# Optimization experiments

Hardware: AMD Instinct MI355X
Metric: run time of the kernel (lower is better)

Reference implementation:

```python
import jax, jax.numpy as jnp
import numpy as np

HEADS = 16
DIM_HEAD = 64
SCALE = DIM_HEAD ** -0.5


def setup_inputs() -> dict:
    key = jax.random.key(0)
    k1, k2, k3, k4 = jax.random.split(key, 4)
    b, n, dim = 2, 2048, 1024
    inner = HEADS * DIM_HEAD  # 1024
    x = jax.random.normal(k1, (b, n, dim), dtype=jnp.float32)
    # binary keep-mask (multiplicative, as in the original module)
    seq_mask = (jax.random.uniform(k2, (b, n)) < 0.9).astype(jnp.float32)
    # weights stored [in, out] (transpose of torch Linear layout)
    w_qkv = jax.random.normal(k3, (dim, inner * 3), dtype=jnp.float32) * (dim ** -0.5)
    w_out = jax.random.normal(k4, (inner, dim), dtype=jnp.float32) * (inner ** -0.5)
    return {"x": x, "seq_mask": seq_mask, "w_qkv": w_qkv, "w_out": w_out}


def reference(x, seq_mask, w_qkv, w_out):
    b, n, dim = x.shape
    qkv = x @ w_qkv                                   # [b, n, 3*inner]
    q, k, v = jnp.split(qkv, 3, axis=-1)
    split_heads = lambda t: t.reshape(b, n, HEADS, DIM_HEAD).transpose(0, 2, 1, 3)
    q, k, v = split_heads(q), split_heads(k), split_heads(v)  # [b, h, n, d]
    dots = jnp.einsum('bhid,bhjd->bhij', q, k) * SCALE        # [b, h, n, n]
    # multiplicative mask, broadcast over heads and query index i; mask depends on key index j
    dots = dots * seq_mask[:, None, None, :]
    attn = jax.nn.softmax(dots, axis=-1)
    out = jnp.einsum('bhij,bhjd->bhid', attn, v)              # [b, h, n, d]
    out = out.transpose(0, 2, 1, 3).reshape(b, n, HEADS * DIM_HEAD)
    return out @ w_out                                        # dropout p=0 -> identity
```

## Files before the change

### kernel.cpp

```cpp
#include <hip/hip_runtime.h>
#include <hip/hip_bf16.h>

using bf16 = __hip_bfloat16;
typedef __attribute__((ext_vector_type(8))) short short8;
typedef __attribute__((ext_vector_type(4))) float floatx4;
typedef __attribute__((ext_vector_type(16))) float floatx16;

#define MFMA_BF16(a, b, c) __builtin_amdgcn_mfma_f32_16x16x32_bf16((a), (b), (c), 0, 0, 0)
#define MFMA32(a, b, c) __builtin_amdgcn_mfma_f32_32x32x16_bf16((a), (b), (c), 0, 0, 0)

__device__ __forceinline__ void gload_lds16(const bf16* g, bf16* l) {
  __builtin_amdgcn_global_load_lds((__attribute__((address_space(1))) void*)g,
                                   (__attribute__((address_space(3))) void*)l,
                                   16, 0, 0);
}

__device__ __forceinline__ unsigned short bfbits(float f) {
  bf16 b = __float2bfloat16(f);
  return *reinterpret_cast<unsigned short*>(&b);
}

__device__ __forceinline__ int swz32(int r) { return (r & 7) ^ ((r >> 3) & 3); }

#define KSCALE 0.18033688011112042f

__global__ __launch_bounds__(256)
void probemask_k(const void* __restrict__ msrc, bf16* __restrict__ dst,
                 int* __restrict__ flag) {
  __shared__ int any;
  const int tid = threadIdx.x;
  if (tid == 0) any = 0;
  __syncthreads();
  const unsigned* mw = (const unsigned*)msrc;
  int bad = 0;
#pragma unroll
  for (int i = 0; i < 4; i++) {
    unsigned w = mw[tid * 4 + i];
    if (w != 0u && w != 0x3F800000u) bad = 1;
  }
  if (bad) atomicOr(&any, 1);
  __syncthreads();
  const int isbf = any;
  if (tid == 0) flag[0] = isbf;
  if (isbf) {
#pragma unroll
    for (int i = 0; i < 2; i++)
      ((int4*)dst)[tid * 2 + i] = ((const int4*)msrc)[tid * 2 + i];
  } else {
#pragma unroll
    for (int i = 0; i < 4; i++) {
      float4 v = ((const float4*)msrc)[tid * 4 + i];
      int o = tid * 16 + i * 4;
      dst[o + 0] = __float2bfloat16(v.x);
      dst[o + 1] = __float2bfloat16(v.y);
      dst[o + 2] = __float2bfloat16(v.z);
      dst[o + 3] = __float2bfloat16(v.w);
    }
  }
}

__global__ __launch_bounds__(256)
void cvt_k(const void* __restrict__ src, bf16* __restrict__ dst, int n,
           const int* __restrict__ flag) {
  if (*flag) return;
  int i = (blockIdx.x * 256 + threadIdx.x) * 4;
  if (i >= n) return;
  float4 v = ((const float4*)src)[i >> 2];
  dst[i + 0] = __float2bfloat16(v.x);
  dst[i + 1] = __float2bfloat16(v.y);
  dst[i + 2] = __float2bfloat16(v.z);
  dst[i + 3] = __float2bfloat16(v.w);
}

__global__ __launch_bounds__(256)
void transpose2_k(const void* __restrict__ in0, bf16* __restrict__ out0,
                  const void* __restrict__ in1, bf16* __restrict__ out1,
                  const int* __restrict__ flag) {
  __shared__ bf16 tile[32][33];
  const int isbf = *flag;
  constexpr int R = 1024;
  const void* in;
  bf16* out;
  int C, bx;
  if (blockIdx.x < 96) { in = in0; out = out0; C = 3072; bx = blockIdx.x * 32; }
  else                 { in = in1; out = out1; C = 1024; bx = (blockIdx.x - 96) * 32; }
  int by = blockIdx.y * 32;
  int tx = threadIdx.x & 31, ty = threadIdx.x >> 5;
#pragma unroll
  for (int i = 0; i < 4; i++) {
    size_t idx = (size_t)(by + ty + i * 8) * C + bx + tx;
    tile[ty + i * 8][tx] =
        isbf ? ((const bf16*)in)[idx] : __float2bfloat16(((const float*)in)[idx]);
  }
  __syncthreads();
#pragma unroll
  for (int i = 0; i < 4; i++)
    out[(size_t)(bx + ty + i * 8) * R + by + tx] = tile[tx][ty + i * 8];
}

template <int MODE>
__global__ __launch_bounds__(256, 2)
void gemm_k(const bf16* __restrict__ A, const bf16* __restrict__ Aalt,
            const bf16* __restrict__ Bt,
            bf16* __restrict__ Qo, bf16* __restrict__ Ko, bf16* __restrict__ Vo,
            void* __restrict__ Co, const bf16* __restrict__ Mk,
            const int* __restrict__ flag) {
  constexpr int K = 1024;
  __shared__ __align__(16) bf16 As[128 * 32];
  __shared__ __align__(16) bf16 Bs[128 * 32];

  const int tid = threadIdx.x;
  const int lane = tid & 63;
  const int wv = tid >> 6;
  const int wm = wv & 1, wn = wv >> 1;
  const int l15 = lane & 15, quad = lane >> 4;

  const int bm = blockIdx.y * 128;
  const int bn = blockIdx.x * 128;

  const int sml = tid >> 2;
  const int sg = (tid & 3) ^ ((sml >> 1) & 3);

  const int isbf = *flag;
  const bf16* Ab = (MODE == 0 && isbf) ? Aalt : A;

  floatx4 acc[4][4] = {};

  for (int k0 = 0; k0 < K; k0 += 32) {
    __syncthreads();
    const bf16* a0 = Ab + (size_t)(bm + sml) * K + k0 + sg * 8;
    gload_lds16(a0, &As[tid * 8]);
    gload_lds16(a0 + (size_t)64 * K, &As[2048 + tid * 8]);
    const bf16* b0 = Bt + (size_t)(bn + sml) * K + k0 + sg * 8;
    gload_lds16(b0, &Bs[tid * 8]);
    gload_lds16(b0 + (size_t)64 * K, &Bs[2048 + tid * 8]);
    __syncthreads();

    short8 af[4], bfr[4];
#pragma unroll
    for (int mi = 0; mi < 4; mi++) {
      int m = wm * 64 + mi * 16 + l15;
      af[mi] = *(const short8*)&As[m * 32 + ((quad ^ ((m >> 1) & 3)) * 8)];
    }
#pragma unroll
    for (int ni = 0; ni < 4; ni++) {
      int n = wn * 64 + ni * 16 + l15;
      bfr[ni] = *(const short8*)&Bs[n * 32 + ((quad ^ ((n >> 1) & 3)) * 8)];
    }
#pragma unroll
    for (int mi = 0; mi < 4; mi++)
#pragma unroll
      for (int ni = 0; ni < 4; ni++)
        acc[mi][ni] = MFMA_BF16(af[mi], bfr[ni], acc[mi][ni]);
  }

#pragma unroll
  for (int mi = 0; mi < 4; mi++) {
    const int row0 = bm + wm * 64 + mi * 16 + quad * 4;
#pragma unroll
    for (int ni = 0; ni < 4; ni++) {
      const int col = bn + wn * 64 + ni * 16 + l15;
      if (MODE == 0) {
        const int sec = col >> 10;
        const int cc = col & 1023;
        const int h = cc >> 6, d = cc & 63;
        const int b_idx = row0 >> 11;
        const int nn0 = row0 & 2047;
        if (sec == 0) {
          bf16* dst = Qo + (size_t)(b_idx * 16 + h) * 131072 + (size_t)nn0 * 64 + d;
#pragma unroll
          for (int r = 0; r < 4; r++) dst[r * 64] = __float2bfloat16(acc[mi][ni][r]);
        } else if (sec == 1) {
          const bf16* mrow = Mk + (size_t)b_idx * 2048 + nn0;
          bf16* dst = Ko + (size_t)(b_idx * 16 + h) * 131072 + (size_t)nn0 * 64 + d;
#pragma unroll
          for (int r = 0; r < 4; r++)
            dst[r * 64] = __float2bfloat16(acc[mi][ni][r] * KSCALE *
                                           __bfloat162float(mrow[r]));
        } else {
          bf16* dst = Vo + (size_t)(b_idx * 16 + h) * 131072 + (size_t)d * 2048 + nn0;
#pragma unroll
          for (int r = 0; r < 4; r++) dst[r] = __float2bfloat16(acc[mi][ni][r]);
        }
      } else {
        if (isbf) {
          bf16* C2 = (bf16*)Co;
#pragma unroll
          for (int r = 0; r < 4; r++)
            C2[(size_t)(row0 + r) * 1024 + col] = __float2bfloat16(acc[mi][ni][r]);
        } else {
          float* C2 = (float*)Co;
#pragma unroll
          for (int r = 0; r < 4; r++)
            C2[(size_t)(row0 + r) * 1024 + col] = acc[mi][ni][r];
        }
      }
    }
  }
}

__global__ __launch_bounds__(256, 2)
void flash_k(const bf16* __restrict__ Q, const bf16* __restrict__ K,
             const bf16* __restrict__ VT, bf16* __restrict__ AO) {
  __shared__ __align__(16) bf16 Ks[2][4096];
  __shared__ __align__(16) bf16 Vs[2][4096];
  __shared__ __align__(16) bf16 Ps[8192];

  const int tid = threadIdx.x;
  const int lane = tid & 63;
  const int w = tid >> 6;
  const int l31 = lane & 31;
  const int l5h = lane >> 5;
  const int sw = swz32(l31);

  const int qt = blockIdx.x & 15;
  const int hl = blockIdx.x >> 4;
  const int b_idx = hl >> 4, h = hl & 15;

  const bf16* Qh = Q + (size_t)hl * 131072;
  const bf16* Kh = K + (size_t)hl * 131072;
  const bf16* Vh = VT + (size_t)hl * 131072;

  const int qbase = qt * 128 + w * 32;
  const int qrow = qbase + l31;

  short8 qf[4];
#pragma unroll
  for (int c = 0; c < 4; c++)
    qf[c] = *(const short8*)&Qh[(size_t)qrow * 64 + c * 16 + l5h * 8];

  floatx16 o_acc[2] = {};
  float rsum = 0.f;

  bf16* Psw = Ps + w * 2048;

  const int sjj = tid >> 3;
  const int sgp = (tid & 7) ^ swz32(sjj);

  gload_lds16(&Kh[(size_t)sjj * 64 + sgp * 8], &Ks[0][tid * 8]);
  gload_lds16(&Kh[(size_t)(32 + sjj) * 64 + sgp * 8], &Ks[0][2048 + tid * 8]);
  gload_lds16(&Vh[(size_t)sjj * 2048 + sgp * 8], &Vs[0][tid * 8]);
  gload_lds16(&Vh[(size_t)(32 + sjj) * 2048 + sgp * 8], &Vs[0][2048 + tid * 8]);

  for (int it = 0; it < 32; ++it) {
    const int b = it & 1;
    __syncthreads();
    if (it < 31) {
      const int j1 = (it + 1) * 64;
      gload_lds16(&Kh[(size_t)(j1 + sjj) * 64 + sgp * 8], &Ks[b ^ 1][tid * 8]);
      gload_lds16(&Kh[(size_t)(j1 + 32 + sjj) * 64 + sgp * 8], &Ks[b ^ 1][2048 + tid * 8]);
      gload_lds16(&Vh[(size_t)sjj * 2048 + j1 + sgp * 8], &Vs[b ^ 1][tid * 8]);
      gload_lds16(&Vh[(size_t)(32 + sjj) * 2048 + j1 + sgp * 8], &Vs[b ^ 1][2048 + tid * 8]);
    }

    floatx16 s[2] = {};
#pragma unroll
    for (int kt = 0; kt < 2; kt++) {
      const int key = kt * 32 + l31;
#pragma unroll
      for (int c = 0; c < 4; c++) {
        const int g = c * 2 + l5h;
        short8 kf = *(const short8*)&Ks[b][key * 64 + ((g ^ sw) * 8)];
        s[kt] = MFMA32(kf, qf[c], s[kt]);
      }
    }

    float rs = 0.f;
#pragma unroll
    for (int kt = 0; kt < 2; kt++)
#pragma unroll
      for (int r = 0; r < 16; r++) {
        const float p = __builtin_amdgcn_exp2f(s[kt][r]);
        s[kt][r] = p;
        rs += p;
      }
    rs += __shfl_xor(rs, 32, 64);
    rsum += rs;

#pragma unroll
    for (int kt = 0; kt < 2; kt++)
#pragma unroll
      for (int rg = 0; rg < 4; rg++) {
        ushort4 u;
        u.x = bfbits(s[kt][rg * 4 + 0]);
        u.y = bfbits(s[kt][rg * 4 + 1]);
        u.z = bfbits(s[kt][rg * 4 + 2]);
        u.w = bfbits(s[kt][rg * 4 + 3]);
        const int g = kt * 4 + rg;
        *(ushort4*)&Psw[l31 * 64 + ((g ^ sw) * 8) + l5h * 4] = u;
      }
    __builtin_amdgcn_wave_barrier();

    short8 pf[4];
#pragma unroll
    for (int c = 0; c < 4; c++) {
      const int g = c * 2 + l5h;
      pf[c] = *(const short8*)&Psw[l31 * 64 + ((g ^ sw) * 8)];
    }

#pragma unroll
    for (int dt = 0; dt < 2; dt++) {
      const int d = dt * 32 + l31;
#pragma unroll
      for (int c = 0; c < 4; c++) {
        const int g = c * 2 + l5h;
        short8 vf = *(const short8*)&Vs[b][d * 64 + ((g ^ sw) * 8)];
        o_acc[dt] = MFMA32(vf, pf[c], o_acc[dt]);
      }
    }
  }

  const float rinv = 1.f / rsum;
  bf16* orow = AO + (size_t)(b_idx * 2048 + qbase + l31) * 1024 + h * 64;
#pragma unroll
  for (int dt = 0; dt < 2; dt++)
#pragma unroll
    for (int rg = 0; rg < 4; rg++) {
      ushort4 u;
      u.x = bfbits(o_acc[dt][rg * 4 + 0] * rinv);
      u.y = bfbits(o_acc[dt][rg * 4 + 1] * rinv);
      u.z = bfbits(o_acc[dt][rg * 4 + 2] * rinv);
      u.w = bfbits(o_acc[dt][rg * 4 + 3] * rinv);
      *(ushort4*)&orow[dt * 32 + rg * 8 + l5h * 4] = u;
    }
}

extern "C" void kernel_launch(void* const* d_in, const int* in_sizes, int n_in,
                              void* d_out, int out_size, void* d_ws, size_t ws_size,
                              hipStream_t stream) {
  const void* x     = d_in[0];
  const void* mask  = d_in[1];
  const void* w_qkv = d_in[2];
  const void* w_out = d_in[3];

  bf16* ws    = (bf16*)d_ws;
  bf16* xb    = ws;
  bf16* AO    = ws;
  bf16* wqkvT = ws + 4194304;
  bf16* woutT = wqkvT + 3145728;
  bf16* Qb    = woutT + 1048576;
  bf16* Kb    = Qb + 4194304;
  bf16* maskb = Kb + 4194304;
  int*  flag  = (int*)(maskb + 4096);
  bf16* VT    = (bf16*)d_out;

  probemask_k<<<1, 256, 0, stream>>>(mask, maskb, flag);
  cvt_k<<<4096, 256, 0, stream>>>(x, xb, 4194304, flag);
  transpose2_k<<<dim3(128, 32), 256, 0, stream>>>(w_qkv, wqkvT, w_out, woutT, flag);
  gemm_k<0><<<dim3(24, 32), 256, 0, stream>>>(xb, (const bf16*)x, wqkvT, Qb, Kb, VT,
                                              nullptr, maskb, flag);
  flash_k<<<512, 256, 0, stream>>>(Qb, Kb, VT, AO);
  gemm_k<1><<<dim3(8, 32), 256, 0, stream>>>(AO, nullptr, woutT, nullptr, nullptr,
                                             nullptr, d_out, nullptr, flag);
}
```

Before: 196.7 us.

## Pack softmax probabilities in registers via permlane swap instead of LDS round-trip

Drops the per-wave shared-memory staging of P. The exp outputs are converted to bf16 with packed cvt instructions and redistributed across lane halves with v_permlane32_swap, so they form the B operand of the PV MFMA directly. This removes LDS writes, reads and a wave barrier per tile and frees 16KB of LDS, which may allow more blocks per CU. It also splits the row-sum into four accumulators and raises wave priority around the MFMA sections; the inline asm relies on gfx950-specific instructions and on the lane layout matching exactly.

```diff
diff --git a/kernel.cpp b/kernel.cpp
--- a/kernel.cpp
+++ b/kernel.cpp
@@ -204,11 +204,9 @@
              const bf16* __restrict__ VT, bf16* __restrict__ AO) {
   __shared__ __align__(16) bf16 Ks[2][4096];
   __shared__ __align__(16) bf16 Vs[2][4096];
-  __shared__ __align__(16) bf16 Ps[8192];
 
   const int tid = threadIdx.x;
   const int lane = tid & 63;
-  const int w = tid >> 6;
   const int l31 = lane & 31;
   const int l5h = lane >> 5;
   const int sw = swz32(l31);
@@ -216,6 +214,7 @@
   const int qt = blockIdx.x & 15;
   const int hl = blockIdx.x >> 4;
   const int b_idx = hl >> 4, h = hl & 15;
+  const int w = tid >> 6;
 
   const bf16* Qh = Q + (size_t)hl * 131072;
   const bf16* Kh = K + (size_t)hl * 131072;
@@ -231,8 +230,6 @@
 
   floatx16 o_acc[2] = {};
   float rsum = 0.f;
-
-  bf16* Psw = Ps + w * 2048;
 
   const int sjj = tid >> 3;
   const int sgp = (tid & 7) ^ swz32(sjj);
@@ -254,6 +251,7 @@
     }
 
     floatx16 s[2] = {};
+    __builtin_amdgcn_s_setprio(1);
 #pragma unroll
     for (int kt = 0; kt < 2; kt++) {
       const int key = kt * 32 + l31;
@@ -264,40 +262,44 @@
         s[kt] = MFMA32(kf, qf[c], s[kt]);
       }
     }
-
-    float rs = 0.f;
+    __builtin_amdgcn_s_setprio(0);
+
+    float rs0 = 0.f, rs1 = 0.f, rs2 = 0.f, rs3 = 0.f;
 #pragma unroll
     for (int kt = 0; kt < 2; kt++)
 #pragma unroll
-      for (int r = 0; r < 16; r++) {
-        const float p = __builtin_amdgcn_exp2f(s[kt][r]);
-        s[kt][r] = p;
-        rs += p;
+      for (int r = 0; r < 16; r += 4) {
+        const float p0 = __builtin_amdgcn_exp2f(s[kt][r + 0]);
+        const float p1 = __builtin_amdgcn_exp2f(s[kt][r + 1]);
+        const float p2 = __builtin_amdgcn_exp2f(s[kt][r + 2]);
+        const float p3 = __builtin_amdgcn_exp2f(s[kt][r + 3]);
+        s[kt][r + 0] = p0; rs0 += p0;
+        s[kt][r + 1] = p1; rs1 += p1;
+        s[kt][r + 2] = p2; rs2 += p2;
+        s[kt][r + 3] = p3; rs3 += p3;
       }
+    float rs = (rs0 + rs1) + (rs2 + rs3);
     rs += __shfl_xor(rs, 32, 64);
     rsum += rs;
 
-#pragma unroll
-    for (int kt = 0; kt < 2; kt++)
-#pragma unroll
-      for (int rg = 0; rg < 4; rg++) {
-        ushort4 u;
-        u.x = bfbits(s[kt][rg * 4 + 0]);
-        u.y = bfbits(s[kt][rg * 4 + 1]);
-        u.z = bfbits(s[kt][rg * 4 + 2]);
-        u.w = bfbits(s[kt][rg * 4 + 3]);
-        const int g = kt * 4 + rg;
-        *(ushort4*)&Psw[l31 * 64 + ((g ^ sw) * 8) + l5h * 4] = u;
-      }
-    __builtin_amdgcn_wave_barrier();
-
     short8 pf[4];
 #pragma unroll
     for (int c = 0; c < 4; c++) {
-      const int g = c * 2 + l5h;
-      pf[c] = *(const short8*)&Psw[l31 * 64 + ((g ^ sw) * 8)];
-    }
-
+      const int kt = c >> 1;
+      const int rb = (c & 1) * 8;
+      unsigned x0, x1, y0, y1;
+      asm("v_cvt_pk_bf16_f32 %0, %1, %2" : "=v"(x0) : "v"(s[kt][rb + 0]), "v"(s[kt][rb + 1]));
+      asm("v_cvt_pk_bf16_f32 %0, %1, %2" : "=v"(x1) : "v"(s[kt][rb + 2]), "v"(s[kt][rb + 3]));
+      asm("v_cvt_pk_bf16_f32 %0, %1, %2" : "=v"(y0) : "v"(s[kt][rb + 4]), "v"(s[kt][rb + 5]));
+      asm("v_cvt_pk_bf16_f32 %0, %1, %2" : "=v"(y1) : "v"(s[kt][rb + 6]), "v"(s[kt][rb + 7]));
+      asm("v_permlane32_swap_b32 %0, %1" : "+v"(x0), "+v"(y0));
+      asm("v_permlane32_swap_b32 %0, %1" : "+v"(x1), "+v"(y1));
+      union { unsigned u[4]; short8 v; } cv;
+      cv.u[0] = x0; cv.u[1] = x1; cv.u[2] = y0; cv.u[3] = y1;
+      pf[c] = cv.v;
+    }
+
+    __builtin_amdgcn_s_setprio(1);
 #pragma unroll
     for (int dt = 0; dt < 2; dt++) {
       const int d = dt * 32 + l31;
@@ -308,6 +310,7 @@
         o_acc[dt] = MFMA32(vf, pf[c], o_acc[dt]);
       }
     }
+    __builtin_amdgcn_s_setprio(0);
   }
 
   const float rinv = 1.f / rsum;
```

Measured after the change: 193.7 us. About the same (-1.5%).
